# Performance work log

Hardware: AMD Instinct MI355X
Metric: run time of the kernel (lower is better)

The kernel has to match this reference:

```python
import jax, jax.numpy as jnp
import numpy as np

N = 100000
E = 1600000
B = 4
IN_C, HID_C, OUT_C = 128, 16, 64
EPS = 1e-5


def _xavier(key, shape):
    fan_in, fan_out = shape[0], shape[1]
    a = float(np.sqrt(6.0 / (fan_in + fan_out)))
    return jax.random.uniform(key, shape, jnp.float32, -a, a)


def setup_inputs() -> dict:
    key = jax.random.key(0)
    ks = jax.random.split(key, 12)
    return {
        "X": jax.random.normal(ks[0], (B, N, IN_C), jnp.float32),
        "edge_index0": jax.random.randint(ks[1], (2, E), 0, N, jnp.int32),
        "edge_weight0": jax.random.uniform(ks[2], (E,), jnp.float32),
        "edge_index1": jax.random.randint(ks[3], (2, E), 0, N, jnp.int32),
        "edge_weight1": jax.random.uniform(ks[4], (E,), jnp.float32),
        "n_id": jnp.arange(N, dtype=jnp.int32),
        "res_n_id0": jnp.arange(N, dtype=jnp.int32),
        "res_n_id1": jnp.arange(N, dtype=jnp.int32),
        # layer 1 params
        "W1_1": _xavier(ks[5], (IN_C, HID_C)),
        "W2_1": _xavier(ks[6], (1, HID_C)),
        "U1": _xavier(ks[7], (HID_C, HID_C)),
        "V1": _xavier(ks[8], (HID_C, HID_C)),
        # layer 2 params
        "W1_2": _xavier(ks[9], (HID_C, OUT_C)),
        "W2_2": _xavier(ks[10], (1, OUT_C)),
        "U2": _xavier(ks[11], (OUT_C, OUT_C)),
        "V2": _xavier(jax.random.fold_in(key, 99), (OUT_C, OUT_C)),
    }


def gated_gcn(x, edge_index, edge_weight, res_n_id, W1, W2, U, V, n_dst):
    # x: [B, N_src, C_in]
    x = x @ W1                                   # [B, N_src, C]
    edge_emb = edge_weight[:, None] * W2[0]      # [E, C]  (edge_feature @ W2)
    src, dst = edge_index[0], edge_index[1]
    msg = edge_emb[None, :, :] * (x[:, src, :] @ V)          # [B, E, C]
    # scatter-mean over destination nodes
    sums = jax.ops.segment_sum(jnp.swapaxes(msg, 0, 1), dst,
                               num_segments=n_dst)            # [N_dst, B, C]
    cnt = jax.ops.segment_sum(jnp.ones((msg.shape[1],), msg.dtype), dst,
                              num_segments=n_dst)
    aggr = jnp.swapaxes(sums, 0, 1) / jnp.maximum(cnt, 1.0)[None, :, None]
    # update
    xr = x[:, res_n_id, :]                       # [B, N_dst, C]
    a = xr @ U + aggr
    # fresh BatchNorm1d(num_features=N_dst) in train mode: normalize each
    # node index over (batch, channel); affine is identity (gamma=1, beta=0)
    mean = jnp.mean(a, axis=(0, 2), keepdims=True)
    var = jnp.var(a, axis=(0, 2), keepdims=True)
    a = jax.nn.relu((a - mean) * jax.lax.rsqrt(var + EPS))
    return xr + a


def reference(X, edge_index0, edge_weight0, edge_index1, edge_weight1,
              n_id, res_n_id0, res_n_id1,
              W1_1, W2_1, U1, V1, W1_2, W2_2, U2, V2):
    X = X[:, n_id, :]
    X = gated_gcn(X, edge_index0, edge_weight0, res_n_id0,
                  W1_1, W2_1, U1, V1, N)
    X = gated_gcn(X, edge_index1, edge_weight1, res_n_id1,
                  W1_2, W2_2, U2, V2, N)
    return X
```

## Files before the change

kernel.cpp:

```cpp
#include <hip/hip_runtime.h>

#define NN 100000
#define EE 1600000
#define EPS 1e-5f
#define NBUK 391
#define NB1 782
#define K1B 6250

typedef __attribute__((ext_vector_type(8))) short short8;
typedef __attribute__((ext_vector_type(4))) float floatx4;
union FragU { uint u[4]; short8 s; };

__device__ __forceinline__ ushort f2bf(float f) {
    uint u = __float_as_uint(f);
    uint r = (u + 0x7FFF + ((u >> 16) & 1)) >> 16;
    return (ushort)r;
}
__device__ __forceinline__ float bf2f(ushort u) {
    return __uint_as_float(((uint)u) << 16);
}

__device__ __forceinline__ int blockScanExcl(int v, int* wsum, int* wpre) {
    int t = threadIdx.x, lane = t & 63, wv = t >> 6;
    int x = v;
#pragma unroll
    for (int off = 1; off < 64; off <<= 1) {
        int y = __shfl_up(x, off, 64);
        if (lane >= off) x += y;
    }
    if (lane == 63) wsum[wv] = x;
    __syncthreads();
    if (t == 0) {
        int ss = 0;
        for (int i = 0; i < 4; ++i) { wpre[i] = ss; ss += wsum[i]; }
    }
    __syncthreads();
    return wpre[wv] + x - v;
}

__device__ __forceinline__ void passC_body(const int* __restrict__ ei, const float* __restrict__ ew,
                                           const int* __restrict__ bhl, const int* __restrict__ gbl,
                                           int2* __restrict__ tl, int b, int* cur) {
    const int* dst = ei + EE;
    int t = threadIdx.x;
    for (int h = t; h < NBUK; h += 256) cur[h] = gbl[h] + bhl[h * NB1 + b];
    __syncthreads();
    long base = (long)b * 2048;
#pragma unroll
    for (int k = 0; k < 8; ++k) {
        long i = base + k * 256 + t;
        if (i < EE) {
            int d = dst[i];
            int slot = atomicAdd(&cur[d >> 8], 1);
            tl[slot] = make_int2(ei[i] | ((d & 255) << 17), __float_as_int(ew[i]));
        }
    }
}

__device__ __forceinline__ void passD_body(const int* __restrict__ gbl, const int2* __restrict__ tl,
                                           int2* __restrict__ ecsr, int* __restrict__ rp,
                                           int h, int* hist, int* wsum, int* wpre) {
    int t = threadIdx.x;
    int base = gbl[h], size = gbl[h + 1] - base;
    hist[t] = 0;
    __syncthreads();
    for (int i = t; i < size; i += 256)
        atomicAdd(&hist[(tl[base + i].x >> 17) & 255], 1);
    __syncthreads();
    int v = hist[t];
    int excl = blockScanExcl(v, wsum, wpre);
    int node = h * 256 + t;
    if (node < NN) rp[node] = base + excl;
    __syncthreads();
    hist[t] = excl;
    __syncthreads();
    for (int i = t; i < size; i += 256) {
        int2 r = tl[base + i];
        int L = (r.x >> 17) & 255;
        int slot = base + atomicAdd(&hist[L], 1);
        ecsr[slot] = make_int2((r.x & 0x1FFFF) << 7, r.y);
    }
}

__global__ __launch_bounds__(256) void kA(const float* __restrict__ X,
                                          const float* __restrict__ W1_1,
                                          ushort* __restrict__ x1g,
                                          const int* __restrict__ ei0,
                                          const int* __restrict__ ei1,
                                          int* __restrict__ bh,
                                          const float* __restrict__ W1_2,
                                          const float* __restrict__ U2,
                                          const float* __restrict__ V2,
                                          const float* __restrict__ W2_2,
                                          const float* __restrict__ U1,
                                          const float* __restrict__ V1,
                                          const float* __restrict__ W2_1,
                                          ushort* __restrict__ pack5a,
                                          ushort* __restrict__ pack5b,
                                          ushort* __restrict__ pack3,
                                          int2* __restrict__ ecsr0, int2* __restrict__ ecsr1,
                                          int* __restrict__ rp0, int* __restrict__ rp1) {
    __shared__ __align__(16) char smem[64 * 132 * 4 + 4096];
    int t = threadIdx.x;
    if (blockIdx.x >= K1B + 2 * NB1) {
        if (blockIdx.x == K1B + 2 * NB1) {
            for (int i = t; i < 1024; i += 256) {
                int k = i >> 6, j = i & 63;
                float su = 0.f, sv = 0.f;
                for (int m = 0; m < 64; ++m) {
                    float wm = W1_2[k * 64 + m];
                    su += wm * U2[m * 64 + j];
                    sv += wm * V2[m * 64 + j];
                }
                sv *= W2_2[j];
                int jt = j >> 4;
                int l1 = (k >> 3) * 16 + (j & 15);
                int l2 = (2 + (k >> 3)) * 16 + (j & 15);
                int e = k & 7;
                pack5a[(jt * 64 + l1) * 8 + e] = f2bf(su);
                pack5a[(jt * 64 + l2) * 8 + e] = f2bf(sv);
                pack5b[(jt * 64 + l1) * 8 + e] = f2bf(W1_2[k * 64 + j]);
                pack5b[(jt * 64 + l2) * 8 + e] = 0;
            }
            if (t < 16) { ecsr0[EE + t] = make_int2(0, 0); ecsr1[EE + t] = make_int2(0, 0); }
            if (t == 16) rp0[NN] = EE;
            if (t == 17) rp1[NN] = EE;
        } else {
            for (int i = t; i < 512; i += 256) {
                int e = i & 7, l = i >> 3;
                int kk = ((l >> 4) & 3) * 8 + e, h = l & 15;
                float v = (kk < 16) ? U1[kk * 16 + h] : V1[(kk - 16) * 16 + h] * W2_1[h];
                pack3[i] = f2bf(v);
            }
        }
        return;
    }
    if (blockIdx.x >= K1B) {
        int bp = blockIdx.x - K1B;
        int l = bp >= NB1;
        int b = bp - l * NB1;
        const int* dst = (l ? ei1 : ei0) + EE;
        int* hist = (int*)smem;
        for (int i = t; i < NBUK; i += 256) hist[i] = 0;
        __syncthreads();
        long base = (long)b * 2048;
#pragma unroll
        for (int k = 0; k < 8; ++k) {
            long i = base + k * 256 + t;
            if (i < EE) atomicAdd(&hist[dst[i] >> 8], 1);
        }
        __syncthreads();
        int* bhl = bh + (long)l * NBUK * NB1;
        for (int h = t; h < NBUK; h += 256) bhl[h * NB1 + b] = hist[h];
        return;
    }
    float (*Xs)[132] = (float(*)[132])smem;
    ushort* Ws = (ushort*)(smem + 64 * 132 * 4);
    int w = t >> 6, lane = t & 63;
    int nb = blockIdx.x * 16;
    for (int i = t; i < 2048; i += 256) {
        int e = i & 7, l = (i >> 3) & 63, s = i >> 9;
        Ws[i] = f2bf(W1_1[(s * 32 + ((l >> 4) & 3) * 8 + e) * 16 + (l & 15)]);
    }
#pragma unroll
    for (int i = 0; i < 8; ++i) {
        int flat = i * 256 + t;
        int n_loc = flat >> 7;
        int b = (flat >> 5) & 3;
        int c4 = (flat & 31) << 2;
        float4 v = *reinterpret_cast<const float4*>(&X[((long)b * NN + (nb + n_loc)) * 128 + c4]);
        *reinterpret_cast<float4*>(&Xs[n_loc * 4 + b][c4]) = v;
    }
    __syncthreads();
    int arow = lane & 15, q = lane >> 4;
    floatx4 acc = {0.f, 0.f, 0.f, 0.f};
#pragma unroll
    for (int s = 0; s < 4; ++s) {
        const float* xp = &Xs[w * 16 + arow][s * 32 + q * 8];
        float4 xa = *reinterpret_cast<const float4*>(xp);
        float4 xb = *reinterpret_cast<const float4*>(xp + 4);
        FragU a;
        a.u[0] = ((uint)f2bf(xa.y) << 16) | f2bf(xa.x);
        a.u[1] = ((uint)f2bf(xa.w) << 16) | f2bf(xa.z);
        a.u[2] = ((uint)f2bf(xb.y) << 16) | f2bf(xb.x);
        a.u[3] = ((uint)f2bf(xb.w) << 16) | f2bf(xb.z);
        short8 bfrag = *reinterpret_cast<const short8*>(&Ws[(s * 64 + lane) * 8]);
        acc = __builtin_amdgcn_mfma_f32_16x16x32_bf16(a.s, bfrag, acc, 0, 0, 0);
    }
    int nw = nb + w * 4;
#pragma unroll
    for (int r = 0; r < 4; ++r) {
        int i = q * 4 + r;
        x1g[(long)(nw + (i >> 2)) * 64 + (i & 3) * 16 + (lane & 15)] = f2bf(acc[r]);
    }
}

__global__ __launch_bounds__(256) void passB(int* __restrict__ bh, int* __restrict__ colsum) {
    int l = blockIdx.x >= NBUK;
    int h = blockIdx.x - l * NBUK;
    int* row = bh + ((long)l * NBUK + h) * NB1;
    int t = threadIdx.x;
    int v[4];
    int s = 0;
    int b0 = t * 4;
#pragma unroll
    for (int j = 0; j < 4; ++j) {
        int b = b0 + j;
        int x = (b < NB1) ? row[b] : 0;
        v[j] = x;
        s += x;
    }
    __shared__ int wsum[4], wpre[4];
    int run = blockScanExcl(s, wsum, wpre);
#pragma unroll
    for (int j = 0; j < 4; ++j) {
        int b = b0 + j;
        if (b < NB1) row[b] = run;
        run += v[j];
    }
    if (t == 255) colsum[l * NBUK + h] = run;
}

__global__ __launch_bounds__(256) void gbscan(const int* __restrict__ colsum, int* __restrict__ gb) {
    int l = blockIdx.x;
    int t = threadIdx.x;
    const int* cs = colsum + l * NBUK;
    int v[2];
    int s = 0;
#pragma unroll
    for (int j = 0; j < 2; ++j) {
        int i = t * 2 + j;
        int x = (i < NBUK) ? cs[i] : 0;
        v[j] = x;
        s += x;
    }
    __shared__ int wsum[4], wpre[4];
    int run = blockScanExcl(s, wsum, wpre);
    int* g = gb + l * 392;
#pragma unroll
    for (int j = 0; j < 2; ++j) {
        int i = t * 2 + j;
        if (i < NBUK) g[i] = run;
        run += v[j];
    }
    if (t == 255) g[NBUK] = run;
}

__global__ __launch_bounds__(256) void passC0(const int* __restrict__ ei0, const float* __restrict__ ew0,
                                              const int* __restrict__ bh, const int* __restrict__ gb,
                                              int2* __restrict__ tmp) {
    __shared__ int cur[NBUK];
    passC_body(ei0, ew0, bh, gb, tmp, blockIdx.x, cur);
}

__global__ __launch_bounds__(256) void fuseDC(const int* __restrict__ gb, int2* __restrict__ tmp,
                                              int2* __restrict__ ecsr0, int* __restrict__ rp0,
                                              const int* __restrict__ ei1, const float* __restrict__ ew1,
                                              const int* __restrict__ bh) {
    __shared__ int sh[NBUK];
    __shared__ int wsum[4], wpre[4];
    if (blockIdx.x < NBUK) {
        passD_body(gb, tmp, ecsr0, rp0, blockIdx.x, sh, wsum, wpre);
    } else {
        passC_body(ei1, ew1, bh + (long)NBUK * NB1, gb + 392, tmp + (long)EE,
                   blockIdx.x - NBUK, sh);
    }
}

__device__ __forceinline__ void k3_body(const ushort* __restrict__ x1g,
                                        const int2* __restrict__ ecsr0,
                                        const int* __restrict__ rp0,
                                        const ushort* __restrict__ pack3,
                                        ushort* __restrict__ h1g,
                                        ushort (*xg)[16][40], int blk) {
    int t = threadIdx.x;
    int w = t >> 6, lane = t & 63;
    int b = lane >> 4;
    int nb = blk * 16 + w * 4;
    const char* xb = (const char*)x1g;
    int lb = lane << 1;
    int s0 = rp0[nb], b1 = rp0[nb + 1], b2 = rp0[nb + 2], b3 = rp0[nb + 3], s4 = rp0[nb + 4];
    float p0 = 0.f, p1 = 0.f, p2 = 0.f, p3 = 0.f;
    int e = s0;
    int efull = s0 + ((s4 - s0) & ~15);
    for (; e < efull; e += 16) {
        int2 r[16];
#pragma unroll
        for (int i = 0; i < 16; ++i) r[i] = ecsr0[e + i];
        float v[16];
#pragma unroll
        for (int i = 0; i < 16; ++i)
            v[i] = bf2f(*(const ushort*)(xb + (uint)r[i].x + lb));
#pragma unroll
        for (int i = 0; i < 16; ++i) {
            int gi = e + i;
            float c = __int_as_float(r[i].y) * v[i];
            p0 += (gi < b1) ? c : 0.f;
            p1 += (gi < b2) ? c : 0.f;
            p2 += (gi < b3) ? c : 0.f;
            p3 += c;
        }
    }
    if (e < s4) {
        int2 r[16];
#pragma unroll
        for (int i = 0; i < 16; ++i) r[i] = ecsr0[e + i];
        float v[16];
#pragma unroll
        for (int i = 0; i < 16; ++i)
            v[i] = bf2f(*(const ushort*)(xb + (uint)r[i].x + lb));
#pragma unroll
        for (int i = 0; i < 16; ++i) {
            int gi = e + i;
            float c = (gi < s4) ? __int_as_float(r[i].y) * v[i] : 0.f;
            p0 += (gi < b1) ? c : 0.f;
            p1 += (gi < b2) ? c : 0.f;
            p2 += (gi < b3) ? c : 0.f;
            p3 += c;
        }
    }
    float a0 = p0, a1 = p1 - p0, a2 = p2 - p1, a3 = p3 - p2;
    int h = lane & 15;
    xg[w][0 * 4 + b][16 + h] = f2bf(a0 / fmaxf((float)(b1 - s0), 1.f));
    xg[w][1 * 4 + b][16 + h] = f2bf(a1 / fmaxf((float)(b2 - b1), 1.f));
    xg[w][2 * 4 + b][16 + h] = f2bf(a2 / fmaxf((float)(b3 - b2), 1.f));
    xg[w][3 * 4 + b][16 + h] = f2bf(a3 / fmaxf((float)(s4 - b3), 1.f));
#pragma unroll
    for (int j = 0; j < 4; ++j)
        xg[w][j * 4 + b][h] = x1g[(long)(nb + j) * 64 + lane];
    short8 afrag = *reinterpret_cast<const short8*>(&xg[w][lane & 15][(lane >> 4) * 8]);
    short8 bfrag = *reinterpret_cast<const short8*>(&pack3[lane * 8]);
    floatx4 a4 = {0.f, 0.f, 0.f, 0.f};
    a4 = __builtin_amdgcn_mfma_f32_16x16x32_bf16(afrag, bfrag, a4, 0, 0, 0);
    float s = 0.f, s2 = 0.f;
#pragma unroll
    for (int r = 0; r < 4; ++r) { s += a4[r]; s2 += a4[r] * a4[r]; }
#pragma unroll
    for (int off = 1; off <= 8; off <<= 1) {
        s += __shfl_xor(s, off, 64);
        s2 += __shfl_xor(s2, off, 64);
    }
    float mean = s * (1.f / 64.f);
    float var = s2 * (1.f / 64.f) - mean * mean;
    float rs = rsqrtf(var + EPS);
    int node = lane >> 4;
#pragma unroll
    for (int r = 0; r < 4; ++r) {
        float xv = bf2f(xg[w][node * 4 + r][lane & 15]);
        float hv = xv + fmaxf((a4[r] - mean) * rs, 0.f);
        h1g[(long)(nb + node) * 64 + r * 16 + (lane & 15)] = f2bf(hv);
    }
}

__global__ __launch_bounds__(256) void fuseKD(const ushort* __restrict__ x1g,
                                              const int2* __restrict__ ecsr0,
                                              const int* __restrict__ rp0,
                                              const ushort* __restrict__ pack3,
                                              ushort* __restrict__ h1g,
                                              const int* __restrict__ gb,
                                              const int2* __restrict__ tmp,
                                              int2* __restrict__ ecsr1,
                                              int* __restrict__ rp1) {
    __shared__ ushort xg[4][16][40];
    __shared__ int hist[256];
    __shared__ int wsum[4], wpre[4];
    if (blockIdx.x < K1B) {
        k3_body(x1g, ecsr0, rp0, pack3, h1g, xg, blockIdx.x);
    } else {
        passD_body(gb + 392, tmp + (long)EE, ecsr1, rp1, blockIdx.x - K1B, hist, wsum, wpre);
    }
}

__global__ __launch_bounds__(256) void k5(const ushort* __restrict__ h1g,
                                          const int2* __restrict__ ecsr1,
                                          const int* __restrict__ rp1,
                                          const ushort* __restrict__ pack5a,
                                          const ushort* __restrict__ pack5b,
                                          float* __restrict__ out) {
    __shared__ ushort hg[4][16][40];
    int t = threadIdx.x;
    int w = t >> 6, lane = t & 63;
    int b = lane >> 4;
    int nb = blockIdx.x * 16 + w * 4;
    const char* hb = (const char*)h1g;
    int lb = lane << 1;
    int s0 = rp1[nb], b1 = rp1[nb + 1], b2 = rp1[nb + 2], b3 = rp1[nb + 3], s4 = rp1[nb + 4];
    float p0 = 0.f, p1 = 0.f, p2 = 0.f, p3 = 0.f;
    int e = s0;
    int efull = s0 + ((s4 - s0) & ~15);
    for (; e < efull; e += 16) {
        int2 r[16];
#pragma unroll
        for (int i = 0; i < 16; ++i) r[i] = ecsr1[e + i];
        float v[16];
#pragma unroll
        for (int i = 0; i < 16; ++i)
            v[i] = bf2f(*(const ushort*)(hb + (uint)r[i].x + lb));
#pragma unroll
        for (int i = 0; i < 16; ++i) {
            int gi = e + i;
            float c = __int_as_float(r[i].y) * v[i];
            p0 += (gi < b1) ? c : 0.f;
            p1 += (gi < b2) ? c : 0.f;
            p2 += (gi < b3) ? c : 0.f;
            p3 += c;
        }
    }
    if (e < s4) {
        int2 r[16];
#pragma unroll
        for (int i = 0; i < 16; ++i) r[i] = ecsr1[e + i];
        float v[16];
#pragma unroll
        for (int i = 0; i < 16; ++i)
            v[i] = bf2f(*(const ushort*)(hb + (uint)r[i].x + lb));
#pragma unroll
        for (int i = 0; i < 16; ++i) {
            int gi = e + i;
            float c = (gi < s4) ? __int_as_float(r[i].y) * v[i] : 0.f;
            p0 += (gi < b1) ? c : 0.f;
            p1 += (gi < b2) ? c : 0.f;
            p2 += (gi < b3) ? c : 0.f;
            p3 += c;
        }
    }
    float a0 = p0, a1 = p1 - p0, a2 = p2 - p1, a3 = p3 - p2;
    int h = lane & 15;
    hg[w][0 * 4 + b][16 + h] = f2bf(a0 / fmaxf((float)(b1 - s0), 1.f));
    hg[w][1 * 4 + b][16 + h] = f2bf(a1 / fmaxf((float)(b2 - b1), 1.f));
    hg[w][2 * 4 + b][16 + h] = f2bf(a2 / fmaxf((float)(b3 - b2), 1.f));
    hg[w][3 * 4 + b][16 + h] = f2bf(a3 / fmaxf((float)(s4 - b3), 1.f));
#pragma unroll
    for (int j = 0; j < 4; ++j)
        hg[w][j * 4 + b][h] = h1g[(long)(nb + j) * 64 + lane];
    short8 afrag = *reinterpret_cast<const short8*>(&hg[w][lane & 15][(lane >> 4) * 8]);
    floatx4 c1[4], c2[4];
#pragma unroll
    for (int jt = 0; jt < 4; ++jt) {
        short8 bb1 = *reinterpret_cast<const short8*>(&pack5a[(jt * 64 + lane) * 8]);
        short8 bb2 = *reinterpret_cast<const short8*>(&pack5b[(jt * 64 + lane) * 8]);
        floatx4 z = {0.f, 0.f, 0.f, 0.f};
        c1[jt] = __builtin_amdgcn_mfma_f32_16x16x32_bf16(afrag, bb1, z, 0, 0, 0);
        c2[jt] = __builtin_amdgcn_mfma_f32_16x16x32_bf16(afrag, bb2, z, 0, 0, 0);
    }
    float s = 0.f, s2 = 0.f;
#pragma unroll
    for (int jt = 0; jt < 4; ++jt)
#pragma unroll
        for (int r = 0; r < 4; ++r) { float a = c1[jt][r]; s += a; s2 += a * a; }
#pragma unroll
    for (int off = 1; off <= 8; off <<= 1) {
        s += __shfl_xor(s, off, 64);
        s2 += __shfl_xor(s2, off, 64);
    }
    float mean = s * (1.f / 256.f);
    float var = s2 * (1.f / 256.f) - mean * mean;
    float rs = rsqrtf(var + EPS);
    int node = lane >> 4;
    long n = nb + node;
#pragma unroll
    for (int r = 0; r < 4; ++r)
#pragma unroll
        for (int jt = 0; jt < 4; ++jt) {
            float norm = (c1[jt][r] - mean) * rs;
            out[((long)r * NN + n) * 64 + jt * 16 + (lane & 15)] = c2[jt][r] + fmaxf(norm, 0.f);
        }
}

extern "C" void kernel_launch(void* const* d_in, const int* in_sizes, int n_in,
                              void* d_out, int out_size, void* d_ws, size_t ws_size,
                              hipStream_t stream) {
    const float* X    = (const float*)d_in[0];
    const int*   ei0  = (const int*)d_in[1];
    const float* ew0  = (const float*)d_in[2];
    const int*   ei1  = (const int*)d_in[3];
    const float* ew1  = (const float*)d_in[4];
    const float* W1_1 = (const float*)d_in[8];
    const float* W2_1 = (const float*)d_in[9];
    const float* U1   = (const float*)d_in[10];
    const float* V1   = (const float*)d_in[11];
    const float* W1_2 = (const float*)d_in[12];
    const float* W2_2 = (const float*)d_in[13];
    const float* U2   = (const float*)d_in[14];
    const float* V2   = (const float*)d_in[15];
    float* out = (float*)d_out;
    char* ws = (char*)d_ws;

    const long MB = 1000000L;
    ushort* x1g   = (ushort*)(ws + 0L);
    ushort* h1g   = (ushort*)(ws + 13 * MB);
    int2*   tmp   = (int2*)(ws + 26 * MB);
    int*    bh    = (int*)(ws + 52 * MB);
    int*    colsum= (int*)(ws + 55 * MB);
    int*    gb    = (int*)(ws + 55 * MB + 4096);
    int*    rp0   = (int*)(ws + 56 * MB);
    int*    rp1   = (int*)(ws + 57 * MB);
    int2*   ecsr0 = (int2*)(ws + 58 * MB);
    int2*   ecsr1 = (int2*)(ws + 71 * MB);
    ushort* pack3  = (ushort*)(ws + 84 * MB);
    ushort* pack5a = (ushort*)(ws + 84 * MB + 8192);
    ushort* pack5b = (ushort*)(ws + 84 * MB + 16384);

    kA<<<K1B + 2 * NB1 + 2, 256, 0, stream>>>(X, W1_1, x1g, ei0, ei1, bh,
                                              W1_2, U2, V2, W2_2, U1, V1, W2_1,
                                              pack5a, pack5b, pack3, ecsr0, ecsr1, rp0, rp1);
    passB<<<2 * NBUK, 256, 0, stream>>>(bh, colsum);
    gbscan<<<2, 256, 0, stream>>>(colsum, gb);
    passC0<<<NB1, 256, 0, stream>>>(ei0, ew0, bh, gb, tmp);
    fuseDC<<<NBUK + NB1, 256, 0, stream>>>(gb, tmp, ecsr0, rp0, ei1, ew1, bh);
    fuseKD<<<K1B + NBUK, 256, 0, stream>>>(x1g, ecsr0, rp0, pack3, h1g, gb, tmp, ecsr1, rp1);
    k5<<<K1B, 256, 0, stream>>>(h1g, ecsr1, rp1, pack5a, pack5b, out);
}
```

Measured before the change: 290.3 us.

## Move layer-1 GEMM into passC kernel and use packed bf16 conversion

Splits the old kA kernel: the histogram and weight-packing blocks now form a small kernel kH. The X@W1_1 MFMA projection moves into the passC0 launch (kGC) so it runs alongside the layer-0 scatter pass. This shortens the critical path through the histogram and scan kernels and lets the bandwidth-heavy GEMM overlap the scatter work. It also replaces the manual float-to-bf16 rounding pairs with the v_cvt_pk_bf16_f32 instruction, at the cost of a larger combined kernel with a bigger LDS footprint on the passC blocks.

Result: no change. 286.3 us (-1.4%).

```diff
diff --git a/kernel.cpp b/kernel.cpp
--- a/kernel.cpp
+++ b/kernel.cpp
@@ -19,6 +19,11 @@
 __device__ __forceinline__ float bf2f(ushort u) {
     return __uint_as_float(((uint)u) << 16);
 }
+__device__ __forceinline__ uint cvtpk(float lo, float hi) {
+    uint r;
+    asm("v_cvt_pk_bf16_f32 %0, %1, %2" : "=v"(r) : "v"(lo), "v"(hi));
+    return r;
+}
 
 __device__ __forceinline__ int blockScanExcl(int v, int* wsum, int* wpre) {
     int t = threadIdx.x, lane = t & 63, wv = t >> 6;
@@ -82,10 +87,7 @@
     }
 }
 
-__global__ __launch_bounds__(256) void kA(const float* __restrict__ X,
-                                          const float* __restrict__ W1_1,
-                                          ushort* __restrict__ x1g,
-                                          const int* __restrict__ ei0,
+__global__ __launch_bounds__(256) void kH(const int* __restrict__ ei0,
                                           const int* __restrict__ ei1,
                                           int* __restrict__ bh,
                                           const float* __restrict__ W1_2,
@@ -100,10 +102,10 @@
                                           ushort* __restrict__ pack3,
                                           int2* __restrict__ ecsr0, int2* __restrict__ ecsr1,
                                           int* __restrict__ rp0, int* __restrict__ rp1) {
-    __shared__ __align__(16) char smem[64 * 132 * 4 + 4096];
-    int t = threadIdx.x;
-    if (blockIdx.x >= K1B + 2 * NB1) {
-        if (blockIdx.x == K1B + 2 * NB1) {
+    __shared__ int hist[NBUK];
+    int t = threadIdx.x;
+    if (blockIdx.x >= 2 * NB1) {
+        if (blockIdx.x == 2 * NB1) {
             for (int i = t; i < 1024; i += 256) {
                 int k = i >> 6, j = i & 63;
                 float su = 0.f, sv = 0.f;
@@ -135,23 +137,84 @@
         }
         return;
     }
+    int l = blockIdx.x >= NB1;
+    int b = blockIdx.x - l * NB1;
+    const int* dst = (l ? ei1 : ei0) + EE;
+    for (int i = t; i < NBUK; i += 256) hist[i] = 0;
+    __syncthreads();
+    long base = (long)b * 2048;
+#pragma unroll
+    for (int k = 0; k < 8; ++k) {
+        long i = base + k * 256 + t;
+        if (i < EE) atomicAdd(&hist[dst[i] >> 8], 1);
+    }
+    __syncthreads();
+    int* bhl = bh + (long)l * NBUK * NB1;
+    for (int h = t; h < NBUK; h += 256) bhl[h * NB1 + b] = hist[h];
+}
+
+__global__ __launch_bounds__(256) void passB(int* __restrict__ bh, int* __restrict__ colsum) {
+    int l = blockIdx.x >= NBUK;
+    int h = blockIdx.x - l * NBUK;
+    int* row = bh + ((long)l * NBUK + h) * NB1;
+    int t = threadIdx.x;
+    int v[4];
+    int s = 0;
+    int b0 = t * 4;
+#pragma unroll
+    for (int j = 0; j < 4; ++j) {
+        int b = b0 + j;
+        int x = (b < NB1) ? row[b] : 0;
+        v[j] = x;
+        s += x;
+    }
+    __shared__ int wsum[4], wpre[4];
+    int run = blockScanExcl(s, wsum, wpre);
+#pragma unroll
+    for (int j = 0; j < 4; ++j) {
+        int b = b0 + j;
+        if (b < NB1) row[b] = run;
+        run += v[j];
+    }
+    if (t == 255) colsum[l * NBUK + h] = run;
+}
+
+__global__ __launch_bounds__(256) void gbscan(const int* __restrict__ colsum, int* __restrict__ gb) {
+    int l = blockIdx.x;
+    int t = threadIdx.x;
+    const int* cs = colsum + l * NBUK;
+    int v[2];
+    int s = 0;
+#pragma unroll
+    for (int j = 0; j < 2; ++j) {
+        int i = t * 2 + j;
+        int x = (i < NBUK) ? cs[i] : 0;
+        v[j] = x;
+        s += x;
+    }
+    __shared__ int wsum[4], wpre[4];
+    int run = blockScanExcl(s, wsum, wpre);
+    int* g = gb + l * 392;
+#pragma unroll
+    for (int j = 0; j < 2; ++j) {
+        int i = t * 2 + j;
+        if (i < NBUK) g[i] = run;
+        run += v[j];
+    }
+    if (t == 255) g[NBUK] = run;
+}
+
+__global__ __launch_bounds__(256) void kGC(const float* __restrict__ X,
+                                           const float* __restrict__ W1_1,
+                                           ushort* __restrict__ x1g,
+                                           const int* __restrict__ ei0, const float* __restrict__ ew0,
+                                           const int* __restrict__ bh, const int* __restrict__ gb,
+                                           int2* __restrict__ tmp) {
+    __shared__ __align__(16) char smem[64 * 132 * 4 + 4096];
+    int t = threadIdx.x;
     if (blockIdx.x >= K1B) {
-        int bp = blockIdx.x - K1B;
-        int l = bp >= NB1;
-        int b = bp - l * NB1;
-        const int* dst = (l ? ei1 : ei0) + EE;
-        int* hist = (int*)smem;
-        for (int i = t; i < NBUK; i += 256) hist[i] = 0;
-        __syncthreads();
-        long base = (long)b * 2048;
-#pragma unroll
-        for (int k = 0; k < 8; ++k) {
-            long i = base + k * 256 + t;
-            if (i < EE) atomicAdd(&hist[dst[i] >> 8], 1);
-        }
-        __syncthreads();
-        int* bhl = bh + (long)l * NBUK * NB1;
-        for (int h = t; h < NBUK; h += 256) bhl[h * NB1 + b] = hist[h];
+        int* cur = (int*)smem;
+        passC_body(ei0, ew0, bh, gb, tmp, blockIdx.x - K1B, cur);
         return;
     }
     float (*Xs)[132] = (float(*)[132])smem;
@@ -180,10 +243,10 @@
         float4 xa = *reinterpret_cast<const float4*>(xp);
         float4 xb = *reinterpret_cast<const float4*>(xp + 4);
         FragU a;
-        a.u[0] = ((uint)f2bf(xa.y) << 16) | f2bf(xa.x);
-        a.u[1] = ((uint)f2bf(xa.w) << 16) | f2bf(xa.z);
-        a.u[2] = ((uint)f2bf(xb.y) << 16) | f2bf(xb.x);
-        a.u[3] = ((uint)f2bf(xb.w) << 16) | f2bf(xb.z);
+        a.u[0] = cvtpk(xa.x, xa.y);
+        a.u[1] = cvtpk(xa.z, xa.w);
+        a.u[2] = cvtpk(xb.x, xb.y);
+        a.u[3] = cvtpk(xb.z, xb.w);
         short8 bfrag = *reinterpret_cast<const short8*>(&Ws[(s * 64 + lane) * 8]);
         acc = __builtin_amdgcn_mfma_f32_16x16x32_bf16(a.s, bfrag, acc, 0, 0, 0);
     }
@@ -193,64 +256,6 @@
         int i = q * 4 + r;
         x1g[(long)(nw + (i >> 2)) * 64 + (i & 3) * 16 + (lane & 15)] = f2bf(acc[r]);
     }
-}
-
-__global__ __launch_bounds__(256) void passB(int* __restrict__ bh, int* __restrict__ colsum) {
-    int l = blockIdx.x >= NBUK;
-    int h = blockIdx.x - l * NBUK;
-    int* row = bh + ((long)l * NBUK + h) * NB1;
-    int t = threadIdx.x;
-    int v[4];
-    int s = 0;
-    int b0 = t * 4;
-#pragma unroll
-    for (int j = 0; j < 4; ++j) {
-        int b = b0 + j;
-        int x = (b < NB1) ? row[b] : 0;
-        v[j] = x;
-        s += x;
-    }
-    __shared__ int wsum[4], wpre[4];
-    int run = blockScanExcl(s, wsum, wpre);
-#pragma unroll
-    for (int j = 0; j < 4; ++j) {
-        int b = b0 + j;
-        if (b < NB1) row[b] = run;
-        run += v[j];
-    }
-    if (t == 255) colsum[l * NBUK + h] = run;
-}
-
-__global__ __launch_bounds__(256) void gbscan(const int* __restrict__ colsum, int* __restrict__ gb) {
-    int l = blockIdx.x;
-    int t = threadIdx.x;
-    const int* cs = colsum + l * NBUK;
-    int v[2];
-    int s = 0;
-#pragma unroll
-    for (int j = 0; j < 2; ++j) {
-        int i = t * 2 + j;
-        int x = (i < NBUK) ? cs[i] : 0;
-        v[j] = x;
-        s += x;
-    }
-    __shared__ int wsum[4], wpre[4];
-    int run = blockScanExcl(s, wsum, wpre);
-    int* g = gb + l * 392;
-#pragma unroll
-    for (int j = 0; j < 2; ++j) {
-        int i = t * 2 + j;
-        if (i < NBUK) g[i] = run;
-        run += v[j];
-    }
-    if (t == 255) g[NBUK] = run;
-}
-
-__global__ __launch_bounds__(256) void passC0(const int* __restrict__ ei0, const float* __restrict__ ew0,
-                                              const int* __restrict__ bh, const int* __restrict__ gb,
-                                              int2* __restrict__ tmp) {
-    __shared__ int cur[NBUK];
-    passC_body(ei0, ew0, bh, gb, tmp, blockIdx.x, cur);
 }
 
 __global__ __launch_bounds__(256) void fuseDC(const int* __restrict__ gb, int2* __restrict__ tmp,
@@ -501,12 +506,11 @@
     ushort* pack5a = (ushort*)(ws + 84 * MB + 8192);
     ushort* pack5b = (ushort*)(ws + 84 * MB + 16384);
 
-    kA<<<K1B + 2 * NB1 + 2, 256, 0, stream>>>(X, W1_1, x1g, ei0, ei1, bh,
-                                              W1_2, U2, V2, W2_2, U1, V1, W2_1,
-                                              pack5a, pack5b, pack3, ecsr0, ecsr1, rp0, rp1);
+    kH<<<2 * NB1 + 2, 256, 0, stream>>>(ei0, ei1, bh, W1_2, U2, V2, W2_2, U1, V1, W2_1,
+                                        pack5a, pack5b, pack3, ecsr0, ecsr1, rp0, rp1);
     passB<<<2 * NBUK, 256, 0, stream>>>(bh, colsum);
     gbscan<<<2, 256, 0, stream>>>(colsum, gb);
-    passC0<<<NB1, 256, 0, stream>>>(ei0, ew0, bh, gb, tmp);
+    kGC<<<K1B + NB1, 256, 0, stream>>>(X, W1_1, x1g, ei0, ew0, bh, gb, tmp);
     fuseDC<<<NBUK + NB1, 256, 0, stream>>>(gb, tmp, ecsr0, rp0, ei1, ew1, bh);
     fuseKD<<<K1B + NBUK, 256, 0, stream>>>(x1g, ecsr0, rp0, pack3, h1g, gb, tmp, ecsr1, rp1);
     k5<<<K1B, 256, 0, stream>>>(h1g, ecsr1, rp1, pack5a, pack5b, out);
```
